# Kernel tuning notes

Measured on AMD Instinct MI355X. Metric: run time of the kernel, lower is better.

## Reference

```python
import jax, jax.numpy as jnp
import numpy as np

N_MENTIONS = 4096
N_PAIRS = 32768
N_SEGMENTS = 1024  # number of spans (ragged softmax groups)
G_DIM = 3 * 768    # span representation dim (3*embed_dim)
D_IN = 3 * G_DIM + 20
HIDDEN = 150


def setup_inputs() -> dict:
    key = jax.random.key(0)
    ks = jax.random.split(key, 11)
    inp = {
        "g_i": jax.random.normal(ks[0], (N_MENTIONS, G_DIM), jnp.float32),
        "mention_scores": jax.random.normal(ks[1], (N_MENTIONS, 1), jnp.float32),
        "speaker_embed": jax.random.normal(ks[2], (3, 20), jnp.float32) * 0.02,
        "W1": jax.random.normal(ks[3], (D_IN, HIDDEN), jnp.float32) * (1.0 / np.sqrt(D_IN)),
        "b1": jnp.zeros((HIDDEN,), jnp.float32),
        "W2": jax.random.normal(ks[4], (HIDDEN, 1), jnp.float32) * (1.0 / np.sqrt(HIDDEN)),
        "b2": jnp.zeros((1,), jnp.float32),
        "mention_ids": jax.random.randint(ks[5], (N_PAIRS,), 0, N_MENTIONS),
        "antecedent_ids": jax.random.randint(ks[6], (N_PAIRS,), 0, N_MENTIONS),
        "speaker_labels": jax.random.randint(ks[7], (N_PAIRS,), 0, 3),
        "segment_ids": jnp.sort(jax.random.randint(ks[8], (N_PAIRS,), 0, N_SEGMENTS)),
    }
    return inp


def reference(g_i, mention_scores, speaker_embed, W1, b1, W2, b2,
              mention_ids, antecedent_ids, speaker_labels, segment_ids):
    # Gather mention / antecedent span representations. [P, G]
    i_g = g_i[mention_ids]
    j_g = g_i[antecedent_ids]
    phi = speaker_embed[speaker_labels]  # [P, speaker_dim]

    # Pair features: cat(i_g, j_g, i_g*j_g, phi). [P, D_IN]
    pairs = jnp.concatenate([i_g, j_g, i_g * j_g, phi], axis=1)

    # Score MLP: Linear -> ReLU -> Linear(->1). (dropout off in eval)
    h = jax.nn.relu(pairs @ W1 + b1)          # [P, HIDDEN]
    s_ij = (h @ W2 + b2)[:, 0]                # [P]

    # coref score = s_i + s_j + s_ij
    s_i = mention_scores[mention_ids, 0]
    s_j = mention_scores[antecedent_ids, 0]
    scores = s_i + s_j + s_ij                 # [P]

    # Ragged per-span softmax with an appended epsilon logit of 0.0.
    seg_max = jax.ops.segment_max(scores, segment_ids, num_segments=N_SEGMENTS)
    m = jnp.maximum(seg_max, 0.0)             # include epsilon=0 in the max
    e = jnp.exp(scores - m[segment_ids])      # [P]
    eps_e = jnp.exp(-m)                       # [S] exp(0 - m)
    denom = jax.ops.segment_sum(e, segment_ids, num_segments=N_SEGMENTS) + eps_e
    pair_probs = e / denom[segment_ids]       # [P]
    eps_probs = eps_e / denom                 # [S]

    # Flattened: all pair probs followed by the per-span epsilon probs.
    return jnp.concatenate([pair_probs, eps_probs])
```

## Files before the change

### kernel.cpp

```cpp
#include <hip/hip_runtime.h>
#include <cstdint>

#define NM   4096
#define NP   32768
#define NSEG 1024
#define GD   2304
#define HID  150
#define NPAD 160
#define KG32 72
#define SEG_ELEMS (KG32 * 10 * 512)

typedef unsigned short u16;
typedef short s16x8 __attribute__((ext_vector_type(8)));
typedef float f32x4 __attribute__((ext_vector_type(4)));
typedef uint32_t u32x4 __attribute__((ext_vector_type(4)));

union Frag {
    uint32_t u[4];
    s16x8    v;
};

__device__ inline uint32_t cvtpk(float lo, float hi) {
    uint32_t r;
    asm("v_cvt_pk_bf16_f32 %0, %1, %2" : "=v"(r) : "v"(lo), "v"(hi));
    return r;
}

__device__ inline f32x4 mfma16(s16x8 a, s16x8 b, f32x4 c) {
    return __builtin_amdgcn_mfma_f32_16x16x32_bf16(a, b, c, 0, 0, 0);
}

__device__ inline s16x8 prodpack(u32x4 iu, u32x4 ju) {
    Frag f;
#pragma unroll
    for (int m = 0; m < 4; ++m) {
        uint32_t x = iu[m], y = ju[m];
        float lo = __builtin_bit_cast(float, x << 16) *
                   __builtin_bit_cast(float, y << 16);
        float hi = __builtin_bit_cast(float, x & 0xffff0000u) *
                   __builtin_bit_cast(float, y & 0xffff0000u);
        f.u[m] = cvtpk(lo, hi);
    }
    return f.v;
}

__launch_bounds__(256)
__global__ void prep_kernel(const float* __restrict__ W1,
                            const float* __restrict__ spk,
                            const float* __restrict__ b1,
                            const float* __restrict__ W2,
                            const int* __restrict__ mids,
                            u16* __restrict__ wpack,
                            float* __restrict__ phib,
                            float* __restrict__ w2pad,
                            int* __restrict__ cnt) {
    const int b = blockIdx.x;
    if (b < 540) {
        int idx = b * 256 + threadIdx.x;
        int lane = idx & 63;
        int t    = idx >> 6;
        int nf   = t % 10;
        int sk   = t / 10;
        int seg  = sk / KG32, kg = sk % KG32;
        int kbase = (seg == 0) ? 2 * GD : ((seg == 1) ? 0 : GD);
        int n    = nf * 16 + (lane & 15);
        int krow = kbase + kg * 32 + ((lane >> 4) << 3);
        u32x4 d = (u32x4){0u, 0u, 0u, 0u};
        if (n < HID) {
#pragma unroll
            for (int jj = 0; jj < 4; ++jj) {
                float v0 = W1[(size_t)(krow + 2 * jj) * HID + n];
                float v1 = W1[(size_t)(krow + 2 * jj + 1) * HID + n];
                d[jj] = cvtpk(v0, v1);
            }
        }
        *(u32x4*)(wpack + (size_t)idx * 8) = d;
    } else if (b < 543) {
        int t = (b - 540) * 256 + threadIdx.x;
        if (t < 3 * NPAD) {
            int s = t / NPAD, n = t - s * NPAD;
            float a = 0.f;
            if (n < HID) {
                for (int d = 0; d < 20; ++d)
                    a = fmaf(spk[s * 20 + d], W1[(size_t)(3 * GD + d) * HID + n], a);
                a += b1[n];
            }
            phib[t] = a;
        } else if (t < 4 * NPAD) {
            int n = t - 3 * NPAD;
            w2pad[n] = (n < HID) ? W2[n] : 0.f;
        }
    } else {
        int p = (b - 543) * 256 + threadIdx.x;
        if (p < NP) atomicAdd(&cnt[mids[p]], 1);
    }
}

__global__ __launch_bounds__(1024)
void sort_scan_kernel(int* __restrict__ cnt, int* __restrict__ bas) {
    __shared__ int lsum[1024];
    const int t = threadIdx.x;
    int v[4];
    int s = 0;
#pragma unroll
    for (int j = 0; j < 4; ++j) { v[j] = cnt[4 * t + j]; s += v[j]; }
    int val = s;
    lsum[t] = val;
    __syncthreads();
    for (int off = 1; off < 1024; off <<= 1) {
        int x = (t >= off) ? lsum[t - off] : 0;
        __syncthreads();
        val += x;
        lsum[t] = val;
        __syncthreads();
    }
    int run = val - s;
#pragma unroll
    for (int j = 0; j < 4; ++j) {
        bas[4 * t + j] = run;
        run += v[j];
        cnt[4 * t + j] = 0;
    }
}

struct A2 { f32x4 x0, x1; };

__launch_bounds__(512, 4)
__global__ void gemm_pre_kernel(const float* __restrict__ gi,
                                const u16* __restrict__ wpackIJ,
                                u16* __restrict__ gbf,
                                float* __restrict__ APre,
                                const int* __restrict__ mids,
                                const int* __restrict__ bas,
                                int* __restrict__ cnt,
                                int* __restrict__ perm) {
    const int blk = blockIdx.x;
    if (blk >= 512) {
        int p = (blk - 512) * 512 + threadIdx.x;
        if (p < NP) {
            int m = mids[p];
            int pos = bas[m] + atomicAdd(&cnt[m], 1);
            perm[pos] = p;
        }
        return;
    }

    __shared__ float xch[7][64][44];

    const int tid = threadIdx.x;
    const int kh = tid >> 6, lane = tid & 63;
    const int quad = lane >> 4, l15 = lane & 15;
    const int mt = blk & 255, ng = blk >> 8;
    const u16* wp = wpackIJ + (size_t)ng * SEG_ELEMS + lane * 8;
    const int row = mt * 16 + l15;

    f32x4 acc[10];
#pragma unroll
    for (int b = 0; b < 10; ++b) acc[b] = (f32x4){0.f, 0.f, 0.f, 0.f};

    const float* ap = gi + (size_t)row * GD + quad * 8;
    u16* gb = gbf + (size_t)row * GD + quad * 8;
    const bool emit = (ng == 0);
    const int u0 = kh * 9;

    A2 a0, a1;
    Frag bE[5], bO[5], apk;

#define LDA(ax, k) { ax.x0 = *(const f32x4*)(ap + (u0 + (k)) * 32); \
                     ax.x1 = *(const f32x4*)(ap + (u0 + (k)) * 32 + 4); }
#define LDB5(bb, k, hf) { const u16* wn = wp + (size_t)(u0 + (k)) * 5120 + (hf) * 2560; \
        _Pragma("unroll") for (int nf = 0; nf < 5; ++nf) \
            bb[nf].v = *(const s16x8*)(const void*)(wn + nf * 512); }
#define PACKA(ax) { \
        apk.u[0] = cvtpk(ax.x0[0], ax.x0[1]); apk.u[1] = cvtpk(ax.x0[2], ax.x0[3]); \
        apk.u[2] = cvtpk(ax.x1[0], ax.x1[1]); apk.u[3] = cvtpk(ax.x1[2], ax.x1[3]); }
#define STEP(s, ax) { \
        PACKA(ax); \
        if (emit) *(u32x4*)(gb + (u0 + (s)) * 32) = *(const u32x4*)apk.u; \
        _Pragma("unroll") for (int nf = 0; nf < 5; ++nf) \
            acc[nf] = mfma16(apk.v, bE[nf].v, acc[nf]); \
        if ((s) < 8) LDB5(bE, (s) + 1, 0); \
        if ((s) < 7) LDA(ax, (s) + 2); \
        _Pragma("unroll") for (int nf = 0; nf < 5; ++nf) \
            acc[5 + nf] = mfma16(apk.v, bO[nf].v, acc[5 + nf]); \
        if ((s) < 8) LDB5(bO, (s) + 1, 1); }

    LDB5(bE, 0, 0); LDB5(bO, 0, 1);
    LDA(a0, 0); LDA(a1, 1);

    STEP(0, a0); STEP(1, a1); STEP(2, a0); STEP(3, a1); STEP(4, a0);
    STEP(5, a1); STEP(6, a0); STEP(7, a1); STEP(8, a0);

#undef LDA
#undef LDB5
#undef PACKA
#undef STEP

    if (kh != 0) {
        float* dst = &xch[kh - 1][lane][0];
#pragma unroll
        for (int nf = 0; nf < 10; ++nf)
            *(f32x4*)(dst + nf * 4) = acc[nf];
    }
    __syncthreads();
    if (kh == 0) {
#pragma unroll
        for (int k = 0; k < 7; ++k) {
            const float* src = &xch[k][lane][0];
#pragma unroll
            for (int nf = 0; nf < 10; ++nf)
                acc[nf] += *(const f32x4*)(src + nf * 4);
        }
        const int colbase = ng * NPAD + l15;
        float* Ap = APre + (size_t)(mt * 16 + quad * 4) * 320 + colbase;
#pragma unroll
        for (int nf = 0; nf < 10; ++nf)
#pragma unroll
            for (int r = 0; r < 4; ++r)
                Ap[(size_t)r * 320 + nf * 16] = acc[nf][r];
    }
}

struct G4 { u32x4 i0, j0, i1, j1; };

__launch_bounds__(128)
__global__ void gemm_pairs_kernel(const u16* __restrict__ gbf,
                                  const u16* __restrict__ wpackP,
                                  const float* __restrict__ APre,
                                  const float* __restrict__ phib,
                                  const float* __restrict__ w2pad,
                                  const float* __restrict__ mscore,
                                  const float* __restrict__ b2,
                                  const int* __restrict__ mids,
                                  const int* __restrict__ aids,
                                  const int* __restrict__ slab,
                                  const int* __restrict__ perm,
                                  float* __restrict__ scores) {
    const int tid = threadIdx.x;
    const int wave = tid >> 6, lane = tid & 63;
    const int quad = lane >> 4, l15 = lane & 15;
    const int base = blockIdx.x * 64 + wave * 32;

    f32x4 acc[2][10];
#pragma unroll
    for (int a = 0; a < 2; ++a)
#pragma unroll
        for (int b = 0; b < 10; ++b) acc[a][b] = (f32x4){0.f, 0.f, 0.f, 0.f};

    const int p0 = perm[base + l15], p1 = perm[base + 16 + l15];
    const u16* ip0 = gbf + (size_t)mids[p0] * GD + quad * 8;
    const u16* jp0 = gbf + (size_t)aids[p0] * GD + quad * 8;
    const u16* ip1 = gbf + (size_t)mids[p1] * GD + quad * 8;
    const u16* jp1 = gbf + (size_t)aids[p1] * GD + quad * 8;
    const u16* wl = wpackP + lane * 8;

    G4 g0, g1, g2;
    Frag b0[10], b1[10];

#define LDG(g, k) { const int off = (k) * 32; \
        g.i0 = *(const u32x4*)(ip0 + off); g.j0 = *(const u32x4*)(jp0 + off); \
        g.i1 = *(const u32x4*)(ip1 + off); g.j1 = *(const u32x4*)(jp1 + off); }
#define LDB(bb, k) { const u16* wn = wl + (size_t)(k) * 5120; \
        _Pragma("unroll") for (int nf = 0; nf < 10; ++nf) \
            bb[nf].v = *(const s16x8*)(const void*)(wn + nf * 512); }
#define PH(g, bb) { \
        s16x8 a0 = prodpack(g.i0, g.j0); \
        s16x8 a1 = prodpack(g.i1, g.j1); \
        _Pragma("unroll") for (int nf = 0; nf < 10; ++nf) { \
            acc[0][nf] = mfma16(a0, bb[nf].v, acc[0][nf]); \
            acc[1][nf] = mfma16(a1, bb[nf].v, acc[1][nf]); } }

    LDG(g0, 0); LDG(g1, 1); LDG(g2, 2);
    LDB(b0, 0); LDB(b1, 1);

#pragma unroll 1
    for (int t = 0; t < 11; ++t) {
        const int kb = t * 6;
        PH(g0, b0); LDG(g0, kb + 3); LDB(b0, kb + 2);
        PH(g1, b1); LDG(g1, kb + 4); LDB(b1, kb + 3);
        PH(g2, b0); LDG(g2, kb + 5); LDB(b0, kb + 4);
        PH(g0, b1); LDG(g0, kb + 6); LDB(b1, kb + 5);
        PH(g1, b0); LDG(g1, kb + 7); LDB(b0, kb + 6);
        PH(g2, b1); LDG(g2, kb + 8); LDB(b1, kb + 7);
    }
    PH(g0, b0); LDG(g0, 69); LDB(b0, 68);
    PH(g1, b1); LDG(g1, 70); LDB(b1, 69);
    PH(g2, b0); LDG(g2, 71); LDB(b0, 70);
    PH(g0, b1); LDB(b1, 71);
    PH(g1, b0);
    PH(g2, b1);

#undef LDG
#undef LDB
#undef PH

    float w2v[10];
#pragma unroll
    for (int nf = 0; nf < 10; ++nf) w2v[nf] = w2pad[nf * 16 + l15];
    const float b2v = b2[0];

#pragma unroll
    for (int mf = 0; mf < 2; ++mf)
#pragma unroll
        for (int r = 0; r < 4; ++r) {
            const int p  = perm[base + mf * 16 + quad * 4 + r];
            const int mi = mids[p], ai = aids[p], sp = slab[p];
            const float* Ai = APre + (size_t)mi * 320;
            const float* Bj = APre + (size_t)ai * 320 + NPAD;
            const float* Ph = phib + sp * NPAD;
            float partial = 0.f;
#pragma unroll
            for (int nf = 0; nf < 10; ++nf) {
                const int c = nf * 16 + l15;
                float h = acc[mf][nf][r] + Ai[c] + Bj[c] + Ph[c];
                h = fmaxf(h, 0.f);
                partial = fmaf(h, w2v[nf], partial);
            }
            partial += __shfl_xor(partial, 1);
            partial += __shfl_xor(partial, 2);
            partial += __shfl_xor(partial, 4);
            partial += __shfl_xor(partial, 8);
            if (l15 == 0)
                scores[p] = partial + b2v + mscore[mi] + mscore[ai];
        }
}

__global__ void seg_softmax_kernel(const float* __restrict__ scores,
                                   const int* __restrict__ seg,
                                   float* __restrict__ out) {
    const int s = blockIdx.x;
    const int lane = threadIdx.x;

    const int tgt = s + (lane & 1);
    int lo = 0, hi = NP;
    while (lo < hi) { int mid = (lo + hi) >> 1; if (seg[mid] < tgt) lo = mid + 1; else hi = mid; }
    const int start = __shfl(lo, 0);
    const int end   = __shfl(lo, 1);

    float m = 0.f;
    for (int i = start + lane; i < end; i += 64) m = fmaxf(m, scores[i]);
#pragma unroll
    for (int msk = 1; msk < 64; msk <<= 1) m = fmaxf(m, __shfl_xor(m, msk));

    float sum = 0.f;
    for (int i = start + lane; i < end; i += 64) sum += __expf(scores[i] - m);
#pragma unroll
    for (int msk = 1; msk < 64; msk <<= 1) sum += __shfl_xor(sum, msk);

    const float epse = __expf(-m);
    const float inv  = 1.f / (sum + epse);
    for (int i = start + lane; i < end; i += 64) out[i] = __expf(scores[i] - m) * inv;
    if (lane == 0) out[NP + s] = epse * inv;
}

extern "C" void kernel_launch(void* const* d_in, const int* in_sizes, int n_in,
                              void* d_out, int out_size, void* d_ws, size_t ws_size,
                              hipStream_t stream) {
    const float* gi     = (const float*)d_in[0];
    const float* mscore = (const float*)d_in[1];
    const float* spk    = (const float*)d_in[2];
    const float* W1     = (const float*)d_in[3];
    const float* b1     = (const float*)d_in[4];
    const float* W2     = (const float*)d_in[5];
    const float* b2     = (const float*)d_in[6];
    const int*   mids   = (const int*)d_in[7];
    const int*   aids   = (const int*)d_in[8];
    const int*   slab   = (const int*)d_in[9];
    const int*   segs   = (const int*)d_in[10];
    float* out = (float*)d_out;

    char* w = (char*)d_ws;
    u16*   gbf    = (u16*)w;
    u16*   wpack  = (u16*)(w + 18874368);
    float* APre   = (float*)(w + 21086208);
    float* scores = (float*)(w + 26329088);
    float* phib   = (float*)(w + 26460160);
    float* w2pad  = (float*)(w + 26462080);
    int*   cnt    = (int*)(w + 26462720);
    int*   bas    = (int*)(w + 26479104);
    int*   perm   = (int*)(w + 26495488);

    hipMemsetAsync(cnt, 0, NM * sizeof(int), stream);
    prep_kernel<<<dim3(671), dim3(256), 0, stream>>>(W1, spk, b1, W2, mids,
                                                     wpack, phib, w2pad, cnt);
    sort_scan_kernel<<<dim3(1), dim3(1024), 0, stream>>>(cnt, bas);
    gemm_pre_kernel<<<dim3(576), dim3(512), 0, stream>>>(gi, wpack + SEG_ELEMS, gbf, APre,
                                                         mids, bas, cnt, perm);
    gemm_pairs_kernel<<<dim3(512), dim3(128), 0, stream>>>(gbf, wpack, APre, phib, w2pad,
                                                           mscore, b2, mids, aids, slab,
                                                           perm, scores);
    seg_softmax_kernel<<<dim3(NSEG), dim3(64), 0, stream>>>(scores, segs, out);
}
```

Before: 218.3 us.

## Split pair GEMM hidden columns across two waves per pair group

Each 32-pair group is now handled by two waves, each computing half of the 160 padded hidden columns (5 of 10 n-fragments), and the block grows to 256 threads. The partial second-layer dot products from the two halves are combined through shared memory after a block barrier. This halves per-wave accumulator and B-fragment registers and doubles the wave count, aiming for more occupancy and latency hiding. The cost is that the gathered A operands (i/j rows and their product) are loaded and computed twice, once per wave, plus an added barrier.

Result: slower. 242.1 us (+10.9%).

```diff
diff --git a/kernel.cpp b/kernel.cpp
--- a/kernel.cpp
+++ b/kernel.cpp
@@ -223,7 +223,7 @@
 
 struct G4 { u32x4 i0, j0, i1, j1; };
 
-__launch_bounds__(128)
+__launch_bounds__(256)
 __global__ void gemm_pairs_kernel(const u16* __restrict__ gbf,
                                   const u16* __restrict__ wpackP,
                                   const float* __restrict__ APre,
@@ -237,36 +237,39 @@
                                   const int* __restrict__ perm,
                                   float* __restrict__ scores) {
     const int tid = threadIdx.x;
-    const int wave = tid >> 6, lane = tid & 63;
+    const int wv = tid >> 6, lane = tid & 63;
+    const int pg = wv >> 1, nh = wv & 1;
     const int quad = lane >> 4, l15 = lane & 15;
-    const int base = blockIdx.x * 64 + wave * 32;
-
-    f32x4 acc[2][10];
+    const int base = blockIdx.x * 64 + pg * 32;
+
+    __shared__ float sm[2][2][4][4];
+
+    f32x4 acc[2][5];
 #pragma unroll
     for (int a = 0; a < 2; ++a)
 #pragma unroll
-        for (int b = 0; b < 10; ++b) acc[a][b] = (f32x4){0.f, 0.f, 0.f, 0.f};
+        for (int b = 0; b < 5; ++b) acc[a][b] = (f32x4){0.f, 0.f, 0.f, 0.f};
 
     const int p0 = perm[base + l15], p1 = perm[base + 16 + l15];
     const u16* ip0 = gbf + (size_t)mids[p0] * GD + quad * 8;
     const u16* jp0 = gbf + (size_t)aids[p0] * GD + quad * 8;
     const u16* ip1 = gbf + (size_t)mids[p1] * GD + quad * 8;
     const u16* jp1 = gbf + (size_t)aids[p1] * GD + quad * 8;
-    const u16* wl = wpackP + lane * 8;
+    const u16* wl = wpackP + nh * 2560 + lane * 8;
 
     G4 g0, g1, g2;
-    Frag b0[10], b1[10];
+    Frag b0[5], b1[5];
 
 #define LDG(g, k) { const int off = (k) * 32; \
         g.i0 = *(const u32x4*)(ip0 + off); g.j0 = *(const u32x4*)(jp0 + off); \
         g.i1 = *(const u32x4*)(ip1 + off); g.j1 = *(const u32x4*)(jp1 + off); }
 #define LDB(bb, k) { const u16* wn = wl + (size_t)(k) * 5120; \
-        _Pragma("unroll") for (int nf = 0; nf < 10; ++nf) \
+        _Pragma("unroll") for (int nf = 0; nf < 5; ++nf) \
             bb[nf].v = *(const s16x8*)(const void*)(wn + nf * 512); }
 #define PH(g, bb) { \
         s16x8 a0 = prodpack(g.i0, g.j0); \
         s16x8 a1 = prodpack(g.i1, g.j1); \
-        _Pragma("unroll") for (int nf = 0; nf < 10; ++nf) { \
+        _Pragma("unroll") for (int nf = 0; nf < 5; ++nf) { \
             acc[0][nf] = mfma16(a0, bb[nf].v, acc[0][nf]); \
             acc[1][nf] = mfma16(a1, bb[nf].v, acc[1][nf]); } }
 
@@ -294,11 +297,12 @@
 #undef LDB
 #undef PH
 
-    float w2v[10];
-#pragma unroll
-    for (int nf = 0; nf < 10; ++nf) w2v[nf] = w2pad[nf * 16 + l15];
+    float w2v[5];
+#pragma unroll
+    for (int nf = 0; nf < 5; ++nf) w2v[nf] = w2pad[nh * 80 + nf * 16 + l15];
     const float b2v = b2[0];
 
+    float part[2][4];
 #pragma unroll
     for (int mf = 0; mf < 2; ++mf)
 #pragma unroll
@@ -310,8 +314,8 @@
             const float* Ph = phib + sp * NPAD;
             float partial = 0.f;
 #pragma unroll
-            for (int nf = 0; nf < 10; ++nf) {
-                const int c = nf * 16 + l15;
+            for (int nf = 0; nf < 5; ++nf) {
+                const int c = nh * 80 + nf * 16 + l15;
                 float h = acc[mf][nf][r] + Ai[c] + Bj[c] + Ph[c];
                 h = fmaxf(h, 0.f);
                 partial = fmaf(h, w2v[nf], partial);
@@ -320,9 +324,23 @@
             partial += __shfl_xor(partial, 2);
             partial += __shfl_xor(partial, 4);
             partial += __shfl_xor(partial, 8);
-            if (l15 == 0)
-                scores[p] = partial + b2v + mscore[mi] + mscore[ai];
+            part[mf][r] = partial;
+            if (nh == 1 && l15 == 0) sm[pg][mf][quad][r] = partial;
         }
+    __syncthreads();
+    if (nh == 0) {
+#pragma unroll
+        for (int mf = 0; mf < 2; ++mf)
+#pragma unroll
+            for (int r = 0; r < 4; ++r) {
+                if (l15 == 0) {
+                    const int p  = perm[base + mf * 16 + quad * 4 + r];
+                    const int mi = mids[p], ai = aids[p];
+                    scores[p] = part[mf][r] + sm[pg][mf][quad][r] + b2v +
+                                mscore[mi] + mscore[ai];
+                }
+            }
+    }
 }
 
 __global__ void seg_softmax_kernel(const float* __restrict__ scores,
@@ -386,7 +404,7 @@
     sort_scan_kernel<<<dim3(1), dim3(1024), 0, stream>>>(cnt, bas);
     gemm_pre_kernel<<<dim3(576), dim3(512), 0, stream>>>(gi, wpack + SEG_ELEMS, gbf, APre,
                                                          mids, bas, cnt, perm);
-    gemm_pairs_kernel<<<dim3(512), dim3(128), 0, stream>>>(gbf, wpack, APre, phib, w2pad,
+    gemm_pairs_kernel<<<dim3(512), dim3(256), 0, stream>>>(gbf, wpack, APre, phib, w2pad,
                                                            mscore, b2, mids, aids, slab,
                                                            perm, scores);
     seg_softmax_kernel<<<dim3(NSEG), dim3(64), 0, stream>>>(scores, segs, out);
```
